# Optimization experiments

Measured on AMD Instinct MI355X. Metric: run time of the kernel, lower is better.

The kernel has to match this reference:

```python
import jax, jax.numpy as jnp
import numpy as np

NUM_HEADS = 16

def setup_inputs() -> dict:
    key = jax.random.key(0)
    k1, k2, k3 = jax.random.split(key, 3)
    B, S, H = 2, 2048, 1024
    x = jax.random.normal(k1, (B, S, H), dtype=jnp.float32)
    w_qkv = jax.random.normal(k2, (H, 3 * H), dtype=jnp.float32) * (1.0 / np.sqrt(H))
    w_out = jax.random.normal(k3, (H, H), dtype=jnp.float32) * (1.0 / np.sqrt(H))
    return {"x": x, "w_qkv": w_qkv, "w_out": w_out}

def reference(x, w_qkv, w_out):
    B, S, H = x.shape
    nh = NUM_HEADS
    dh = H // nh
    qkv = x @ w_qkv  # (B, S, 3H)
    q, k, v = jnp.split(qkv, 3, axis=-1)
    # (B, nh, S, dh)
    q = q.reshape(B, S, nh, dh).transpose(0, 2, 1, 3)
    k = k.reshape(B, S, nh, dh).transpose(0, 2, 1, 3)
    v = v.reshape(B, S, nh, dh).transpose(0, 2, 1, 3)
    att = jnp.einsum('bhsd,bhSd->bhsS', q, k) / np.sqrt(dh).astype(np.float32)
    causal = jnp.tril(jnp.ones((S, S), dtype=bool))
    att = jnp.where(causal[None, None], att, -jnp.inf)
    att = jax.nn.softmax(att, axis=-1)
    out = jnp.einsum('bhsS,bhSd->bhsd', att, v)
    out = out.transpose(0, 2, 1, 3).reshape(B, S, H)
    return out @ w_out
```

## Files before the change

### kernel.cpp

```cpp
#include <hip/hip_runtime.h>

#define DEVINL __device__ __forceinline__

typedef __attribute__((ext_vector_type(8)))  __bf16         bf16x8;
typedef __attribute__((ext_vector_type(4)))  float          f32x4;
typedef __attribute__((ext_vector_type(16))) float          f32x16;
typedef __attribute__((ext_vector_type(8)))  unsigned short ushort8;
typedef __attribute__((ext_vector_type(4)))  unsigned short ushort4v;
typedef __attribute__((ext_vector_type(4)))  unsigned int   uint4v;
typedef __attribute__((ext_vector_type(4)))  float          float4v;

DEVINL unsigned short f2bf(float f) {
  unsigned int u = __float_as_uint(f);
  u += 0x7fffu + ((u >> 16) & 1u);
  return (unsigned short)(u >> 16);
}

DEVINL float bf2f(unsigned short u) {
  return __uint_as_float(((unsigned int)u) << 16);
}

DEVINL bf16x8 ldbf8(const unsigned short* p) {
  return __builtin_bit_cast(bf16x8, *(const ushort8*)p);
}

DEVINL unsigned cvtpk_bf16(float lo, float hi) {
  unsigned r;
  asm("v_cvt_pk_bf16_f32 %0, %1, %2" : "=v"(r) : "v"(lo), "v"(hi));
  return r;
}

DEVINL void gload_lds16(const unsigned short* g, unsigned short* l) {
  __builtin_amdgcn_global_load_lds((const __attribute__((address_space(1))) void*)g,
                                   (__attribute__((address_space(3))) void*)l, 16, 0, 0);
}

__global__ __launch_bounds__(256) void prepass_kernel(
    const float* __restrict__ x, const float* __restrict__ w_qkv,
    const float* __restrict__ w_out, unsigned short* __restrict__ xb,
    unsigned short* __restrict__ wqkvT, unsigned short* __restrict__ woutT) {
  __shared__ float tile[32][33];
  const int B = blockIdx.x;
  if (B < 1024) {
    const int n4 = 1048576;
    for (int i = B * 256 + threadIdx.x; i < n4; i += 1024 * 256) {
      float4v v = *(const float4v*)(x + (size_t)4 * i);
      ushort4v o;
      o[0] = f2bf(v[0]); o[1] = f2bf(v[1]); o[2] = f2bf(v[2]); o[3] = f2bf(v[3]);
      *(ushort4v*)(xb + (size_t)4 * i) = o;
    }
    return;
  }
  const float* in; unsigned short* out; int C, bx, by;
  if (B < 4096) { const int idx = B - 1024; bx = idx % 96; by = idx / 96; in = w_qkv; out = wqkvT; C = 3072; }
  else          { const int idx = B - 4096; bx = idx & 31; by = idx >> 5; in = w_out; out = woutT; C = 1024; }
  const int R = 1024;
  const int tx = threadIdx.x & 31, ty = threadIdx.x >> 5;
  const int r0 = by << 5, c0 = bx << 5;
#pragma unroll
  for (int i = 0; i < 32; i += 8)
    tile[ty + i][tx] = in[(size_t)(r0 + ty + i) * C + (c0 + tx)];
  __syncthreads();
#pragma unroll
  for (int i = 0; i < 32; i += 8)
    out[(size_t)(c0 + ty + i) * R + (r0 + tx)] = f2bf(tile[tx][ty + i]);
}

template <bool OUT_BF16>
__global__ __launch_bounds__(256, 3) void gemm_bt_kernel(
    const unsigned short* __restrict__ A,
    const unsigned short* __restrict__ Bt,
    void* __restrict__ Cout,
    int M, int N, int K, int lda, int ldb, int ldc,
    unsigned short* __restrict__ VtOut) {
  __shared__ __align__(16) unsigned short As[2][128 * 32];
  __shared__ __align__(16) unsigned short Bs[2][128 * 32];
  const int tid = threadIdx.x;
  const int lane = tid & 63, wave = tid >> 6;
  const int wr = wave >> 1, wc = wave & 1;
  const int g = lane >> 4, q = lane & 15;
  const int row0 = blockIdx.x << 7, col0 = blockIdx.y << 7;

  const int srow = tid >> 2;
  const int sg = ((tid & 3) ^ (srow & 3)) << 3;
  const unsigned short* Ap0 = A + (size_t)(row0 + srow) * lda + sg;
  const unsigned short* Ap1 = Ap0 + (size_t)64 * lda;
  const unsigned short* Bp0 = Bt + (size_t)(col0 + srow) * ldb + sg;
  const unsigned short* Bp1 = Bp0 + (size_t)64 * ldb;

  f32x4 acc[4][4] = {};

  gload_lds16(Ap0, &As[0][wave * 512]);
  gload_lds16(Ap1, &As[0][2048 + wave * 512]);
  gload_lds16(Bp0, &Bs[0][wave * 512]);
  gload_lds16(Bp1, &Bs[0][2048 + wave * 512]);

  const int gx = (g ^ (q & 3)) << 3;
  const int nk = K >> 5;
  int cur = 0;

  for (int t = 0; t < nk; ++t) {
    if (t + 1 < nk) {
      Ap0 += 32; Ap1 += 32; Bp0 += 32; Bp1 += 32;
      gload_lds16(Ap0, &As[cur ^ 1][wave * 512]);
      gload_lds16(Ap1, &As[cur ^ 1][2048 + wave * 512]);
      gload_lds16(Bp0, &Bs[cur ^ 1][wave * 512]);
      gload_lds16(Bp1, &Bs[cur ^ 1][2048 + wave * 512]);
      asm volatile("s_waitcnt vmcnt(4)" ::: "memory");
    } else {
      asm volatile("s_waitcnt vmcnt(0)" ::: "memory");
    }
    __builtin_amdgcn_s_barrier();

    bf16x8 af[4], bfr[4];
#pragma unroll
    for (int mb = 0; mb < 4; ++mb)
      af[mb] = ldbf8(&As[cur][(wr * 64 + mb * 16 + q) * 32] + gx);
#pragma unroll
    for (int nb = 0; nb < 4; ++nb)
      bfr[nb] = ldbf8(&Bs[cur][(wc * 64 + nb * 16 + q) * 32] + gx);
#pragma unroll
    for (int mb = 0; mb < 4; ++mb)
#pragma unroll
      for (int nb = 0; nb < 4; ++nb)
        acc[mb][nb] = __builtin_amdgcn_mfma_f32_16x16x32_bf16(af[mb], bfr[nb], acc[mb][nb], 0, 0, 0);

    __builtin_amdgcn_s_barrier();
    cur ^= 1;
  }

  const bool isV = OUT_BF16 && (VtOut != nullptr) && (col0 >= 2048);
#pragma unroll
  for (int mb = 0; mb < 4; ++mb)
#pragma unroll
    for (int nb = 0; nb < 4; ++nb)
#pragma unroll
      for (int r = 0; r < 4; ++r) {
        const int row = row0 + wr * 64 + mb * 16 + g * 4 + r;
        const int col = col0 + wc * 64 + nb * 16 + q;
        const float v = acc[mb][nb][r];
        if (isV) {
          const int cp = col - 2048, hI = cp >> 6, dI = cp & 63;
          VtOut[((size_t)((row >> 11) * 16 + hI) * 64 + dI) * 2048 + (row & 2047)] = f2bf(v);
        } else if (OUT_BF16) {
          ((unsigned short*)Cout)[(size_t)row * ldc + col] = f2bf(v);
        } else {
          ((float*)Cout)[(size_t)row * ldc + col] = v;
        }
      }
}

__global__ __launch_bounds__(256, 3) void gemm_bt64_kernel(
    const unsigned short* __restrict__ A,
    const unsigned short* __restrict__ Bt,
    float* __restrict__ Cout,
    int K, int lda, int ldb, int ldc) {
  __shared__ __align__(16) unsigned short As[2][64 * 32];
  __shared__ __align__(16) unsigned short Bs[2][128 * 32];
  const int tid = threadIdx.x;
  const int lane = tid & 63, wave = tid >> 6;
  const int wr = wave >> 1, wc = wave & 1;
  const int g = lane >> 4, q = lane & 15;
  const int row0 = blockIdx.x << 6, col0 = blockIdx.y << 7;

  const int srow = tid >> 2;
  const int sg = ((tid & 3) ^ (srow & 3)) << 3;
  const unsigned short* Ap = A + (size_t)(row0 + srow) * lda + sg;
  const unsigned short* Bp0 = Bt + (size_t)(col0 + srow) * ldb + sg;
  const unsigned short* Bp1 = Bp0 + (size_t)64 * ldb;

  f32x4 acc[2][4] = {};

  gload_lds16(Ap, &As[0][wave * 512]);
  gload_lds16(Bp0, &Bs[0][wave * 512]);
  gload_lds16(Bp1, &Bs[0][2048 + wave * 512]);

  const int gx = (g ^ (q & 3)) << 3;
  const int nk = K >> 5;
  int cur = 0;

  for (int t = 0; t < nk; ++t) {
    if (t + 1 < nk) {
      Ap += 32; Bp0 += 32; Bp1 += 32;
      gload_lds16(Ap, &As[cur ^ 1][wave * 512]);
      gload_lds16(Bp0, &Bs[cur ^ 1][wave * 512]);
      gload_lds16(Bp1, &Bs[cur ^ 1][2048 + wave * 512]);
      asm volatile("s_waitcnt vmcnt(3)" ::: "memory");
    } else {
      asm volatile("s_waitcnt vmcnt(0)" ::: "memory");
    }
    __builtin_amdgcn_s_barrier();

    bf16x8 af[2], bfr[4];
#pragma unroll
    for (int mb = 0; mb < 2; ++mb)
      af[mb] = ldbf8(&As[cur][(wr * 32 + mb * 16 + q) * 32] + gx);
#pragma unroll
    for (int nb = 0; nb < 4; ++nb)
      bfr[nb] = ldbf8(&Bs[cur][(wc * 64 + nb * 16 + q) * 32] + gx);
#pragma unroll
    for (int mb = 0; mb < 2; ++mb)
#pragma unroll
      for (int nb = 0; nb < 4; ++nb)
        acc[mb][nb] = __builtin_amdgcn_mfma_f32_16x16x32_bf16(af[mb], bfr[nb], acc[mb][nb], 0, 0, 0);

    __builtin_amdgcn_s_barrier();
    cur ^= 1;
  }

#pragma unroll
  for (int mb = 0; mb < 2; ++mb)
#pragma unroll
    for (int nb = 0; nb < 4; ++nb)
#pragma unroll
      for (int r = 0; r < 4; ++r) {
        const int row = row0 + wr * 32 + mb * 16 + g * 4 + r;
        const int col = col0 + wc * 64 + nb * 16 + q;
        Cout[(size_t)row * ldc + col] = acc[mb][nb][r];
      }
}

__global__ __launch_bounds__(256, 2) void attn_kernel(
    const unsigned short* __restrict__ qkv,
    const unsigned short* __restrict__ VtG,
    unsigned short* __restrict__ OlP,
    unsigned short* __restrict__ OhP,
    float* __restrict__ stats) {
  const int S = 2048, H = 1024, LD = 2048;
  const int tid = threadIdx.x;
  const int wave = tid >> 6, lane = tid & 63;
  const int c = lane & 31, hh = lane >> 5;

  const int L = blockIdx.x;
  const int group = L >> 8, r0_ = L & 255;
  const int pairid = r0_ & 7, bh = r0_ >> 3;
  const int qc = (group & 2) ? (15 - pairid) : pairid;
  const int half = group & 1;
  const int b = bh >> 4, h = bh & 15;
  const int q0w = qc * 128 + wave * 32;

  const unsigned short* Qb = qkv + (size_t)b * S * LD + h * 64;
  const unsigned short* Kb = Qb + 1024;
  const unsigned short* Vt = VtG + (size_t)(b * 16 + h) * 64 * S;

  __shared__ __align__(16) unsigned short Ks[2][64 * 64];
  __shared__ __align__(16) unsigned short Vs[2][64 * 64];

  const int srow = lane >> 3;
  const int srcg = ((lane & 7) ^ srow) << 3;
  const int wrow = wave * 8 + srow;

  const int nit = qc + 1;
  const int tb = half ? nit : 0;

  {
    const int cc = tb << 6;
    gload_lds16(Kb + (size_t)(cc + wrow) * LD + srcg,      Ks[0] + wave * 512);
    gload_lds16(Kb + (size_t)(cc + 32 + wrow) * LD + srcg, Ks[0] + 2048 + wave * 512);
    gload_lds16(Vt + (size_t)wrow * S + cc + srcg,         Vs[0] + wave * 512);
    gload_lds16(Vt + (size_t)(32 + wrow) * S + cc + srcg,  Vs[0] + 2048 + wave * 512);
  }

  bf16x8 qf[4];
#pragma unroll
  for (int kc = 0; kc < 4; ++kc)
    qf[kc] = ldbf8(Qb + (size_t)(q0w + c) * LD + kc * 16 + hh * 8);

  f32x16 acc[2] = {};
  float m_r = -1e30f, l_r = 0.f;
  const float CE = 0.125f * 1.44269504f;

  int cur = 0;
  const int swz = (c & 7) << 3;

  for (int t = 0; t < nit; ++t) {
    if (t + 1 < nit) {
      const int c1 = (tb + t + 1) << 6;
      unsigned short* KsN = Ks[cur ^ 1];
      unsigned short* VsN = Vs[cur ^ 1];
      gload_lds16(Kb + (size_t)(c1 + wrow) * LD + srcg,      KsN + wave * 512);
      gload_lds16(Kb + (size_t)(c1 + 32 + wrow) * LD + srcg, KsN + 2048 + wave * 512);
      gload_lds16(Vt + (size_t)wrow * S + c1 + srcg,         VsN + wave * 512);
      gload_lds16(Vt + (size_t)(32 + wrow) * S + c1 + srcg,  VsN + 2048 + wave * 512);
      asm volatile("s_waitcnt vmcnt(4)" ::: "memory");
    } else {
      asm volatile("s_waitcnt vmcnt(0)" ::: "memory");
    }
    __builtin_amdgcn_s_barrier();

    const int c0 = (tb + t) << 6;
    const unsigned short* KsC = Ks[cur];
    const unsigned short* VsC = Vs[cur];

    if (c0 <= q0w + 31) {
      int nv = ((q0w + 31 - c0) >> 5) + 1; if (nv > 2) nv = 2;

      bf16x8 kf[2][4];
#pragma unroll
      for (int n = 0; n < 2; ++n) if (n < nv)
#pragma unroll
        for (int kc = 0; kc < 4; ++kc)
          kf[n][kc] = ldbf8(KsC + (n * 32 + c) * 64 + ((kc * 16 + hh * 8) ^ swz));

      f32x16 st[2] = {};
      __builtin_amdgcn_s_setprio(1);
#pragma unroll
      for (int n = 0; n < 2; ++n) if (n < nv)
#pragma unroll
        for (int kc = 0; kc < 4; ++kc)
          st[n] = __builtin_amdgcn_mfma_f32_32x32x16_bf16(kf[n][kc], qf[kc], st[n], 0, 0, 0);
      __builtin_amdgcn_s_setprio(0);

      bf16x8 vf[2][4];
#pragma unroll
      for (int db = 0; db < 2; ++db)
#pragma unroll
        for (int kk = 0; kk < 4; ++kk) if (kk < 2 * nv)
          vf[db][kk] = ldbf8(VsC + (db * 32 + c) * 64 + ((kk * 16 + hh * 8) ^ swz));

      if (c0 + 63 > q0w) {
#pragma unroll
        for (int n = 0; n < 2; ++n) if (n < nv)
#pragma unroll
          for (int r = 0; r < 16; ++r) {
            const int kv = c0 + n * 32 + (r & 3) + 8 * (r >> 2) + 4 * hh;
            if (kv > q0w + c) st[n][r] = -1e30f;
          }
      }

      f32x4 pm = {-1e30f, -1e30f, -1e30f, -1e30f};
#pragma unroll
      for (int n = 0; n < 2; ++n) if (n < nv)
#pragma unroll
        for (int r = 0; r < 16; ++r) pm[r & 3] = fmaxf(pm[r & 3], st[n][r]);
      const float pmax = fmaxf(fmaxf(pm[0], pm[1]), fmaxf(pm[2], pm[3]));
      if (!__all(pmax <= m_r + 64.f)) {
        float px = fmaxf(pmax, __shfl_xor(pmax, 32));
        const float mn = fmaxf(m_r, px);
        const float sf = __builtin_amdgcn_exp2f((m_r - mn) * CE);
        m_r = mn; l_r *= sf;
#pragma unroll
        for (int db = 0; db < 2; ++db) acc[db] *= sf;
      }
      const float mC = m_r * CE;
      f32x4 la = {0.f, 0.f, 0.f, 0.f};
#pragma unroll
      for (int n = 0; n < 2; ++n) if (n < nv)
#pragma unroll
        for (int r = 0; r < 16; ++r) {
          const float p = __builtin_amdgcn_exp2f(fmaf(st[n][r], CE, -mC));
          st[n][r] = p;
          la[r & 3] += p;
        }
      l_r += (la[0] + la[1]) + (la[2] + la[3]);

      bf16x8 pa[4];
#pragma unroll
      for (int n = 0; n < 2; ++n) if (n < nv) {
        unsigned T0 = cvtpk_bf16(st[n][0],  st[n][1]);
        unsigned T1 = cvtpk_bf16(st[n][2],  st[n][3]);
        unsigned T2 = cvtpk_bf16(st[n][4],  st[n][5]);
        unsigned T3 = cvtpk_bf16(st[n][6],  st[n][7]);
        unsigned T4 = cvtpk_bf16(st[n][8],  st[n][9]);
        unsigned T5 = cvtpk_bf16(st[n][10], st[n][11]);
        unsigned T6 = cvtpk_bf16(st[n][12], st[n][13]);
        unsigned T7 = cvtpk_bf16(st[n][14], st[n][15]);
        asm("v_permlane32_swap_b32 %0, %1" : "+v"(T0), "+v"(T2));
        asm("v_permlane32_swap_b32 %0, %1" : "+v"(T1), "+v"(T3));
        asm("v_permlane32_swap_b32 %0, %1" : "+v"(T4), "+v"(T6));
        asm("v_permlane32_swap_b32 %0, %1" : "+v"(T5), "+v"(T7));
        uint4v w0; w0[0] = T0; w0[1] = T1; w0[2] = T2; w0[3] = T3;
        uint4v w1; w1[0] = T4; w1[1] = T5; w1[2] = T6; w1[3] = T7;
        pa[2 * n]     = __builtin_bit_cast(bf16x8, w0);
        pa[2 * n + 1] = __builtin_bit_cast(bf16x8, w1);
      }

      __builtin_amdgcn_s_setprio(1);
#pragma unroll
      for (int kk = 0; kk < 4; ++kk) if (kk < 2 * nv)
#pragma unroll
        for (int db = 0; db < 2; ++db)
          acc[db] = __builtin_amdgcn_mfma_f32_32x32x16_bf16(vf[db][kk], pa[kk], acc[db], 0, 0, 0);
      __builtin_amdgcn_s_setprio(0);
    }

    __builtin_amdgcn_s_barrier();
    cur ^= 1;
  }

  const float lt = l_r + __shfl_xor(l_r, 32);
  const float inv = lt > 0.f ? 1.f / lt : 0.f;
  unsigned short* Op = half ? OhP : OlP;
  const size_t rowbase = (size_t)(b * S + q0w + c) * H + h * 64;
#pragma unroll
  for (int db = 0; db < 2; ++db)
#pragma unroll
    for (int blk = 0; blk < 4; ++blk) {
      ushort4v o;
#pragma unroll
      for (int j = 0; j < 4; ++j) o[j] = f2bf(acc[db][blk * 4 + j] * inv);
      *(ushort4v*)(Op + rowbase + db * 32 + blk * 8 + hh * 4) = o;
    }
  if (hh == 0) {
    float* sp = stats + ((((size_t)(b * 16 + h)) << 11) + q0w + c) * 4 + (half ? 2 : 0);
    sp[0] = m_r; sp[1] = lt;
  }
}

__global__ __launch_bounds__(256) void attn_merge_kernel(
    const unsigned short* __restrict__ Ol,
    const unsigned short* __restrict__ Oh,
    const float* __restrict__ stats,
    unsigned short* __restrict__ Oout) {
  const float CE = 0.125f * 1.44269504f;
  const int i = blockIdx.x * 256 + threadIdx.x;
  const int r = i >> 7;
  const int g8 = i & 127;
  const int h = g8 >> 3;
  const int s = r & 2047, b = r >> 11;
  const float4v st = *(const float4v*)(stats + ((((size_t)(b * 16 + h)) << 11) + s) * 4);
  const float mn = fmaxf(st[0], st[2]);
  const float wl_ = st[1] * __builtin_amdgcn_exp2f((st[0] - mn) * CE);
  const float wh_ = st[3] * __builtin_amdgcn_exp2f((st[2] - mn) * CE);
  const float inv = 1.f / (wl_ + wh_);
  const float wl = wl_ * inv, wh = wh_ * inv;
  const size_t off = (size_t)i * 8;
  const ushort8 a = *(const ushort8*)(Ol + off);
  const ushort8 cc = *(const ushort8*)(Oh + off);
  ushort8 o;
#pragma unroll
  for (int j = 0; j < 8; ++j)
    o[j] = f2bf(wl * bf2f(a[j]) + wh * bf2f(cc[j]));
  *(ushort8*)(Oout + off) = o;
}

extern "C" void kernel_launch(void* const* d_in, const int* in_sizes, int n_in,
                              void* d_out, int out_size, void* d_ws, size_t ws_size,
                              hipStream_t stream) {
  const float* x     = (const float*)d_in[0];
  const float* w_qkv = (const float*)d_in[1];
  const float* w_out = (const float*)d_in[2];
  const int B = 2, S = 2048, H = 1024;
  const int M = B * S;

  unsigned short* xb    = (unsigned short*)d_ws;
  unsigned short* wqkvT = xb + (size_t)M * H;
  unsigned short* woutT = wqkvT + (size_t)3 * H * H;
  unsigned short* qkb   = woutT + (size_t)H * H;
  unsigned short* VtG   = qkb + (size_t)M * 2048;
  unsigned short* Ob    = VtG + (size_t)B * 16 * 64 * S;
  unsigned short* OhP   = xb;
  float*          stats = (float*)wqkvT;

  prepass_kernel<<<5120, 256, 0, stream>>>(x, w_qkv, w_out, xb, wqkvT, woutT);

  gemm_bt_kernel<true><<<dim3(M / 128, (3 * H) / 128), 256, 0, stream>>>(
      xb, wqkvT, qkb, M, 3 * H, H, H, H, 2048, VtG);

  attn_kernel<<<1024, 256, 0, stream>>>(qkb, VtG, Ob, OhP, stats);

  attn_merge_kernel<<<2048, 256, 0, stream>>>(Ob, OhP, stats, Ob);

  gemm_bt64_kernel<<<dim3(M / 64, H / 128), 256, 0, stream>>>(
      Ob, woutT, (float*)d_out, H, H, H, H);
}
```

Baseline: 116.6 us.

## Load attention K/V fragments directly from global and shrink QKV GEMM tile

The attention kernel stops staging K and V tiles through double-buffered LDS with barriers. Each wave now reads its K and V MFMA fragments straight from global memory and skips fully masked tiles through a tighter loop bound. The QKV projection GEMM switches to the 64-row tile variant, which is merged with the output GEMM into one templated kernel; this doubles the grid and lowers per-block register and LDS use. The trade-off is redundant global/L2 traffic in attention, since waves no longer share K/V tiles, and smaller GEMM tiles that get less operand reuse.

```diff
diff --git a/kernel.cpp b/kernel.cpp
--- a/kernel.cpp
+++ b/kernel.cpp
@@ -67,31 +67,29 @@
 }
 
 template <bool OUT_BF16>
-__global__ __launch_bounds__(256, 3) void gemm_bt_kernel(
+__global__ __launch_bounds__(256, 3) void gemm_bt64_kernel(
     const unsigned short* __restrict__ A,
     const unsigned short* __restrict__ Bt,
     void* __restrict__ Cout,
-    int M, int N, int K, int lda, int ldb, int ldc,
+    int K, int lda, int ldb, int ldc,
     unsigned short* __restrict__ VtOut) {
-  __shared__ __align__(16) unsigned short As[2][128 * 32];
+  __shared__ __align__(16) unsigned short As[2][64 * 32];
   __shared__ __align__(16) unsigned short Bs[2][128 * 32];
   const int tid = threadIdx.x;
   const int lane = tid & 63, wave = tid >> 6;
   const int wr = wave >> 1, wc = wave & 1;
   const int g = lane >> 4, q = lane & 15;
-  const int row0 = blockIdx.x << 7, col0 = blockIdx.y << 7;
+  const int row0 = blockIdx.x << 6, col0 = blockIdx.y << 7;
 
   const int srow = tid >> 2;
   const int sg = ((tid & 3) ^ (srow & 3)) << 3;
-  const unsigned short* Ap0 = A + (size_t)(row0 + srow) * lda + sg;
-  const unsigned short* Ap1 = Ap0 + (size_t)64 * lda;
+  const unsigned short* Ap = A + (size_t)(row0 + srow) * lda + sg;
   const unsigned short* Bp0 = Bt + (size_t)(col0 + srow) * ldb + sg;
   const unsigned short* Bp1 = Bp0 + (size_t)64 * ldb;
 
-  f32x4 acc[4][4] = {};
-
-  gload_lds16(Ap0, &As[0][wave * 512]);
-  gload_lds16(Ap1, &As[0][2048 + wave * 512]);
+  f32x4 acc[2][4] = {};
+
+  gload_lds16(Ap, &As[0][wave * 512]);
   gload_lds16(Bp0, &Bs[0][wave * 512]);
   gload_lds16(Bp1, &Bs[0][2048 + wave * 512]);
 
@@ -101,26 +99,25 @@
 
   for (int t = 0; t < nk; ++t) {
     if (t + 1 < nk) {
-      Ap0 += 32; Ap1 += 32; Bp0 += 32; Bp1 += 32;
-      gload_lds16(Ap0, &As[cur ^ 1][wave * 512]);
-      gload_lds16(Ap1, &As[cur ^ 1][2048 + wave * 512]);
+      Ap += 32; Bp0 += 32; Bp1 += 32;
+      gload_lds16(Ap, &As[cur ^ 1][wave * 512]);
       gload_lds16(Bp0, &Bs[cur ^ 1][wave * 512]);
       gload_lds16(Bp1, &Bs[cur ^ 1][2048 + wave * 512]);
-      asm volatile("s_waitcnt vmcnt(4)" ::: "memory");
+      asm volatile("s_waitcnt vmcnt(3)" ::: "memory");
     } else {
       asm volatile("s_waitcnt vmcnt(0)" ::: "memory");
     }
     __builtin_amdgcn_s_barrier();
 
-    bf16x8 af[4], bfr[4];
-#pragma unroll
-    for (int mb = 0; mb < 4; ++mb)
-      af[mb] = ldbf8(&As[cur][(wr * 64 + mb * 16 + q) * 32] + gx);
+    bf16x8 af[2], bfr[4];
+#pragma unroll
+    for (int mb = 0; mb < 2; ++mb)
+      af[mb] = ldbf8(&As[cur][(wr * 32 + mb * 16 + q) * 32] + gx);
 #pragma unroll
     for (int nb = 0; nb < 4; ++nb)
       bfr[nb] = ldbf8(&Bs[cur][(wc * 64 + nb * 16 + q) * 32] + gx);
 #pragma unroll
-    for (int mb = 0; mb < 4; ++mb)
+    for (int mb = 0; mb < 2; ++mb)
 #pragma unroll
       for (int nb = 0; nb < 4; ++nb)
         acc[mb][nb] = __builtin_amdgcn_mfma_f32_16x16x32_bf16(af[mb], bfr[nb], acc[mb][nb], 0, 0, 0);
@@ -131,12 +128,12 @@
 
   const bool isV = OUT_BF16 && (VtOut != nullptr) && (col0 >= 2048);
 #pragma unroll
-  for (int mb = 0; mb < 4; ++mb)
+  for (int mb = 0; mb < 2; ++mb)
 #pragma unroll
     for (int nb = 0; nb < 4; ++nb)
 #pragma unroll
       for (int r = 0; r < 4; ++r) {
-        const int row = row0 + wr * 64 + mb * 16 + g * 4 + r;
+        const int row = row0 + wr * 32 + mb * 16 + g * 4 + r;
         const int col = col0 + wc * 64 + nb * 16 + q;
         const float v = acc[mb][nb][r];
         if (isV) {
@@ -150,76 +147,6 @@
       }
 }
 
-__global__ __launch_bounds__(256, 3) void gemm_bt64_kernel(
-    const unsigned short* __restrict__ A,
-    const unsigned short* __restrict__ Bt,
-    float* __restrict__ Cout,
-    int K, int lda, int ldb, int ldc) {
-  __shared__ __align__(16) unsigned short As[2][64 * 32];
-  __shared__ __align__(16) unsigned short Bs[2][128 * 32];
-  const int tid = threadIdx.x;
-  const int lane = tid & 63, wave = tid >> 6;
-  const int wr = wave >> 1, wc = wave & 1;
-  const int g = lane >> 4, q = lane & 15;
-  const int row0 = blockIdx.x << 6, col0 = blockIdx.y << 7;
-
-  const int srow = tid >> 2;
-  const int sg = ((tid & 3) ^ (srow & 3)) << 3;
-  const unsigned short* Ap = A + (size_t)(row0 + srow) * lda + sg;
-  const unsigned short* Bp0 = Bt + (size_t)(col0 + srow) * ldb + sg;
-  const unsigned short* Bp1 = Bp0 + (size_t)64 * ldb;
-
-  f32x4 acc[2][4] = {};
-
-  gload_lds16(Ap, &As[0][wave * 512]);
-  gload_lds16(Bp0, &Bs[0][wave * 512]);
-  gload_lds16(Bp1, &Bs[0][2048 + wave * 512]);
-
-  const int gx = (g ^ (q & 3)) << 3;
-  const int nk = K >> 5;
-  int cur = 0;
-
-  for (int t = 0; t < nk; ++t) {
-    if (t + 1 < nk) {
-      Ap += 32; Bp0 += 32; Bp1 += 32;
-      gload_lds16(Ap, &As[cur ^ 1][wave * 512]);
-      gload_lds16(Bp0, &Bs[cur ^ 1][wave * 512]);
-      gload_lds16(Bp1, &Bs[cur ^ 1][2048 + wave * 512]);
-      asm volatile("s_waitcnt vmcnt(3)" ::: "memory");
-    } else {
-      asm volatile("s_waitcnt vmcnt(0)" ::: "memory");
-    }
-    __builtin_amdgcn_s_barrier();
-
-    bf16x8 af[2], bfr[4];
-#pragma unroll
-    for (int mb = 0; mb < 2; ++mb)
-      af[mb] = ldbf8(&As[cur][(wr * 32 + mb * 16 + q) * 32] + gx);
-#pragma unroll
-    for (int nb = 0; nb < 4; ++nb)
-      bfr[nb] = ldbf8(&Bs[cur][(wc * 64 + nb * 16 + q) * 32] + gx);
-#pragma unroll
-    for (int mb = 0; mb < 2; ++mb)
-#pragma unroll
-      for (int nb = 0; nb < 4; ++nb)
-        acc[mb][nb] = __builtin_amdgcn_mfma_f32_16x16x32_bf16(af[mb], bfr[nb], acc[mb][nb], 0, 0, 0);
-
-    __builtin_amdgcn_s_barrier();
-    cur ^= 1;
-  }
-
-#pragma unroll
-  for (int mb = 0; mb < 2; ++mb)
-#pragma unroll
-    for (int nb = 0; nb < 4; ++nb)
-#pragma unroll
-      for (int r = 0; r < 4; ++r) {
-        const int row = row0 + wr * 32 + mb * 16 + g * 4 + r;
-        const int col = col0 + wc * 64 + nb * 16 + q;
-        Cout[(size_t)row * ldc + col] = acc[mb][nb][r];
-      }
-}
-
 __global__ __launch_bounds__(256, 2) void attn_kernel(
     const unsigned short* __restrict__ qkv,
     const unsigned short* __restrict__ VtG,
@@ -243,23 +170,9 @@
   const unsigned short* Kb = Qb + 1024;
   const unsigned short* Vt = VtG + (size_t)(b * 16 + h) * 64 * S;
 
-  __shared__ __align__(16) unsigned short Ks[2][64 * 64];
-  __shared__ __align__(16) unsigned short Vs[2][64 * 64];
-
-  const int srow = lane >> 3;
-  const int srcg = ((lane & 7) ^ srow) << 3;
-  const int wrow = wave * 8 + srow;
-
   const int nit = qc + 1;
   const int tb = half ? nit : 0;
-
-  {
-    const int cc = tb << 6;
-    gload_lds16(Kb + (size_t)(cc + wrow) * LD + srcg,      Ks[0] + wave * 512);
-    gload_lds16(Kb + (size_t)(cc + 32 + wrow) * LD + srcg, Ks[0] + 2048 + wave * 512);
-    gload_lds16(Vt + (size_t)wrow * S + cc + srcg,         Vs[0] + wave * 512);
-    gload_lds16(Vt + (size_t)(32 + wrow) * S + cc + srcg,  Vs[0] + 2048 + wave * 512);
-  }
+  const int te = min(tb + nit, ((q0w + 31) >> 6) + 1);
 
   bf16x8 qf[4];
 #pragma unroll
@@ -270,122 +183,97 @@
   float m_r = -1e30f, l_r = 0.f;
   const float CE = 0.125f * 1.44269504f;
 
-  int cur = 0;
-  const int swz = (c & 7) << 3;
-
-  for (int t = 0; t < nit; ++t) {
-    if (t + 1 < nit) {
-      const int c1 = (tb + t + 1) << 6;
-      unsigned short* KsN = Ks[cur ^ 1];
-      unsigned short* VsN = Vs[cur ^ 1];
-      gload_lds16(Kb + (size_t)(c1 + wrow) * LD + srcg,      KsN + wave * 512);
-      gload_lds16(Kb + (size_t)(c1 + 32 + wrow) * LD + srcg, KsN + 2048 + wave * 512);
-      gload_lds16(Vt + (size_t)wrow * S + c1 + srcg,         VsN + wave * 512);
-      gload_lds16(Vt + (size_t)(32 + wrow) * S + c1 + srcg,  VsN + 2048 + wave * 512);
-      asm volatile("s_waitcnt vmcnt(4)" ::: "memory");
-    } else {
-      asm volatile("s_waitcnt vmcnt(0)" ::: "memory");
-    }
-    __builtin_amdgcn_s_barrier();
-
-    const int c0 = (tb + t) << 6;
-    const unsigned short* KsC = Ks[cur];
-    const unsigned short* VsC = Vs[cur];
-
-    if (c0 <= q0w + 31) {
-      int nv = ((q0w + 31 - c0) >> 5) + 1; if (nv > 2) nv = 2;
-
-      bf16x8 kf[2][4];
+  for (int t = tb; t < te; ++t) {
+    const int c0 = t << 6;
+    int nv = ((q0w + 31 - c0) >> 5) + 1; if (nv > 2) nv = 2;
+
+    bf16x8 kf[2][4];
+#pragma unroll
+    for (int n = 0; n < 2; ++n) if (n < nv)
+#pragma unroll
+      for (int kc = 0; kc < 4; ++kc)
+        kf[n][kc] = ldbf8(Kb + (size_t)(c0 + n * 32 + c) * LD + kc * 16 + hh * 8);
+
+    bf16x8 vf[2][4];
+#pragma unroll
+    for (int db = 0; db < 2; ++db)
+#pragma unroll
+      for (int kk = 0; kk < 4; ++kk) if (kk < 2 * nv)
+        vf[db][kk] = ldbf8(Vt + (size_t)(db * 32 + c) * S + c0 + kk * 16 + hh * 8);
+
+    f32x16 st[2] = {};
+    __builtin_amdgcn_s_setprio(1);
+#pragma unroll
+    for (int n = 0; n < 2; ++n) if (n < nv)
+#pragma unroll
+      for (int kc = 0; kc < 4; ++kc)
+        st[n] = __builtin_amdgcn_mfma_f32_32x32x16_bf16(kf[n][kc], qf[kc], st[n], 0, 0, 0);
+    __builtin_amdgcn_s_setprio(0);
+
+    if (c0 + 63 > q0w) {
 #pragma unroll
       for (int n = 0; n < 2; ++n) if (n < nv)
 #pragma unroll
-        for (int kc = 0; kc < 4; ++kc)
-          kf[n][kc] = ldbf8(KsC + (n * 32 + c) * 64 + ((kc * 16 + hh * 8) ^ swz));
-
-      f32x16 st[2] = {};
-      __builtin_amdgcn_s_setprio(1);
-#pragma unroll
-      for (int n = 0; n < 2; ++n) if (n < nv)
-#pragma unroll
-        for (int kc = 0; kc < 4; ++kc)
-          st[n] = __builtin_amdgcn_mfma_f32_32x32x16_bf16(kf[n][kc], qf[kc], st[n], 0, 0, 0);
-      __builtin_amdgcn_s_setprio(0);
-
-      bf16x8 vf[2][4];
+        for (int r = 0; r < 16; ++r) {
+          const int kv = c0 + n * 32 + (r & 3) + 8 * (r >> 2) + 4 * hh;
+          if (kv > q0w + c) st[n][r] = -1e30f;
+        }
+    }
+
+    f32x4 pm = {-1e30f, -1e30f, -1e30f, -1e30f};
+#pragma unroll
+    for (int n = 0; n < 2; ++n) if (n < nv)
+#pragma unroll
+      for (int r = 0; r < 16; ++r) pm[r & 3] = fmaxf(pm[r & 3], st[n][r]);
+    const float pmax = fmaxf(fmaxf(pm[0], pm[1]), fmaxf(pm[2], pm[3]));
+    if (!__all(pmax <= m_r + 64.f)) {
+      float px = fmaxf(pmax, __shfl_xor(pmax, 32));
+      const float mn = fmaxf(m_r, px);
+      const float sf = __builtin_amdgcn_exp2f((m_r - mn) * CE);
+      m_r = mn; l_r *= sf;
+#pragma unroll
+      for (int db = 0; db < 2; ++db) acc[db] *= sf;
+    }
+    const float mC = m_r * CE;
+    f32x4 la = {0.f, 0.f, 0.f, 0.f};
+#pragma unroll
+    for (int n = 0; n < 2; ++n) if (n < nv)
+#pragma unroll
+      for (int r = 0; r < 16; ++r) {
+        const float p = __builtin_amdgcn_exp2f(fmaf(st[n][r], CE, -mC));
+        st[n][r] = p;
+        la[r & 3] += p;
+      }
+    l_r += (la[0] + la[1]) + (la[2] + la[3]);
+
+    bf16x8 pa[4];
+#pragma unroll
+    for (int n = 0; n < 2; ++n) if (n < nv) {
+      unsigned T0 = cvtpk_bf16(st[n][0],  st[n][1]);
+      unsigned T1 = cvtpk_bf16(st[n][2],  st[n][3]);
+      unsigned T2 = cvtpk_bf16(st[n][4],  st[n][5]);
+      unsigned T3 = cvtpk_bf16(st[n][6],  st[n][7]);
+      unsigned T4 = cvtpk_bf16(st[n][8],  st[n][9]);
+      unsigned T5 = cvtpk_bf16(st[n][10], st[n][11]);
+      unsigned T6 = cvtpk_bf16(st[n][12], st[n][13]);
+      unsigned T7 = cvtpk_bf16(st[n][14], st[n][15]);
+      asm("v_permlane32_swap_b32 %0, %1" : "+v"(T0), "+v"(T2));
+      asm("v_permlane32_swap_b32 %0, %1" : "+v"(T1), "+v"(T3));
+      asm("v_permlane32_swap_b32 %0, %1" : "+v"(T4), "+v"(T6));
+      asm("v_permlane32_swap_b32 %0, %1" : "+v"(T5), "+v"(T7));
+      uint4v w0; w0[0] = T0; w0[1] = T1; w0[2] = T2; w0[3] = T3;
+      uint4v w1; w1[0] = T4; w1[1] = T5; w1[2] = T6; w1[3] = T7;
+      pa[2 * n]     = __builtin_bit_cast(bf16x8, w0);
+      pa[2 * n + 1] = __builtin_bit_cast(bf16x8, w1);
+    }
+
+    __builtin_amdgcn_s_setprio(1);
+#pragma unroll
+    for (int kk = 0; kk < 4; ++kk) if (kk < 2 * nv)
 #pragma unroll
       for (int db = 0; db < 2; ++db)
-#pragma unroll
-        for (int kk = 0; kk < 4; ++kk) if (kk < 2 * nv)
-          vf[db][kk] = ldbf8(VsC + (db * 32 + c) * 64 + ((kk * 16 + hh * 8) ^ swz));
-
-      if (c0 + 63 > q0w) {
-#pragma unroll
-        for (int n = 0; n < 2; ++n) if (n < nv)
-#pragma unroll
-          for (int r = 0; r < 16; ++r) {
-            const int kv = c0 + n * 32 + (r & 3) + 8 * (r >> 2) + 4 * hh;
-            if (kv > q0w + c) st[n][r] = -1e30f;
-          }
-      }
-
-      f32x4 pm = {-1e30f, -1e30f, -1e30f, -1e30f};
-#pragma unroll
-      for (int n = 0; n < 2; ++n) if (n < nv)
-#pragma unroll
-        for (int r = 0; r < 16; ++r) pm[r & 3] = fmaxf(pm[r & 3], st[n][r]);
-      const float pmax = fmaxf(fmaxf(pm[0], pm[1]), fmaxf(pm[2], pm[3]));
-      if (!__all(pmax <= m_r + 64.f)) {
-        float px = fmaxf(pmax, __shfl_xor(pmax, 32));
-        const float mn = fmaxf(m_r, px);
-        const float sf = __builtin_amdgcn_exp2f((m_r - mn) * CE);
-        m_r = mn; l_r *= sf;
-#pragma unroll
-        for (int db = 0; db < 2; ++db) acc[db] *= sf;
-      }
-      const float mC = m_r * CE;
-      f32x4 la = {0.f, 0.f, 0.f, 0.f};
-#pragma unroll
-      for (int n = 0; n < 2; ++n) if (n < nv)
-#pragma unroll
-        for (int r = 0; r < 16; ++r) {
-          const float p = __builtin_amdgcn_exp2f(fmaf(st[n][r], CE, -mC));
-          st[n][r] = p;
-          la[r & 3] += p;
-        }
-      l_r += (la[0] + la[1]) + (la[2] + la[3]);
-
-      bf16x8 pa[4];
-#pragma unroll
-      for (int n = 0; n < 2; ++n) if (n < nv) {
-        unsigned T0 = cvtpk_bf16(st[n][0],  st[n][1]);
-        unsigned T1 = cvtpk_bf16(st[n][2],  st[n][3]);
-        unsigned T2 = cvtpk_bf16(st[n][4],  st[n][5]);
-        unsigned T3 = cvtpk_bf16(st[n][6],  st[n][7]);
-        unsigned T4 = cvtpk_bf16(st[n][8],  st[n][9]);
-        unsigned T5 = cvtpk_bf16(st[n][10], st[n][11]);
-        unsigned T6 = cvtpk_bf16(st[n][12], st[n][13]);
-        unsigned T7 = cvtpk_bf16(st[n][14], st[n][15]);
-        asm("v_permlane32_swap_b32 %0, %1" : "+v"(T0), "+v"(T2));
-        asm("v_permlane32_swap_b32 %0, %1" : "+v"(T1), "+v"(T3));
-        asm("v_permlane32_swap_b32 %0, %1" : "+v"(T4), "+v"(T6));
-        asm("v_permlane32_swap_b32 %0, %1" : "+v"(T5), "+v"(T7));
-        uint4v w0; w0[0] = T0; w0[1] = T1; w0[2] = T2; w0[3] = T3;
-        uint4v w1; w1[0] = T4; w1[1] = T5; w1[2] = T6; w1[3] = T7;
-        pa[2 * n]     = __builtin_bit_cast(bf16x8, w0);
-        pa[2 * n + 1] = __builtin_bit_cast(bf16x8, w1);
-      }
-
-      __builtin_amdgcn_s_setprio(1);
-#pragma unroll
-      for (int kk = 0; kk < 4; ++kk) if (kk < 2 * nv)
-#pragma unroll
-        for (int db = 0; db < 2; ++db)
-          acc[db] = __builtin_amdgcn_mfma_f32_32x32x16_bf16(vf[db][kk], pa[kk], acc[db], 0, 0, 0);
-      __builtin_amdgcn_s_setprio(0);
-    }
-
-    __builtin_amdgcn_s_barrier();
-    cur ^= 1;
+        acc[db] = __builtin_amdgcn_mfma_f32_32x32x16_bf16(vf[db][kk], pa[kk], acc[db], 0, 0, 0);
+    __builtin_amdgcn_s_setprio(0);
   }
 
   const float lt = l_r + __shfl_xor(l_r, 32);
@@ -454,13 +342,13 @@
 
   prepass_kernel<<<5120, 256, 0, stream>>>(x, w_qkv, w_out, xb, wqkvT, woutT);
 
-  gemm_bt_kernel<true><<<dim3(M / 128, (3 * H) / 128), 256, 0, stream>>>(
-      xb, wqkvT, qkb, M, 3 * H, H, H, H, 2048, VtG);
+  gemm_bt64_kernel<true><<<dim3(M / 64, (3 * H) / 128), 256, 0, stream>>>(
+      xb, wqkvT, qkb, H, H, H, 2048, VtG);
 
   attn_kernel<<<1024, 256, 0, stream>>>(qkb, VtG, Ob, OhP, stats);
 
   attn_merge_kernel<<<2048, 256, 0, stream>>>(Ob, OhP, stats, Ob);
 
-  gemm_bt64_kernel<<<dim3(M / 64, H / 128), 256, 0, stream>>>(
-      Ob, woutT, (float*)d_out, H, H, H, H);
-}
+  gemm_bt64_kernel<false><<<dim3(M / 64, H / 128), 256, 0, stream>>>(
+      Ob, woutT, d_out, H, H, H, H, nullptr);
+}
```

Result: slower. 158.9 us (+36.3%).

## Split causal attention KV range into four partials with heavy-first block order

Applied to the files above, without the earlier changes.

Attention blocks now split each query chunk's KV tiles into four quarters instead of two halves. The grid doubles to 2048 blocks and is ordered so the longest causal chunks are scheduled first. The merge kernel now combines four partial outputs using per-quarter max and sum stats, with two of the partial buffers placed in the not-yet-written output buffer. This is meant to cut tail imbalance and raise CU occupancy. In exchange, the merge kernel reads twice as many partial buffers, and some blocks do no work for short chunks.

```diff
diff --git a/kernel.cpp b/kernel.cpp
--- a/kernel.cpp
+++ b/kernel.cpp
@@ -223,8 +223,8 @@
 __global__ __launch_bounds__(256, 2) void attn_kernel(
     const unsigned short* __restrict__ qkv,
     const unsigned short* __restrict__ VtG,
-    unsigned short* __restrict__ OlP,
-    unsigned short* __restrict__ OhP,
+    unsigned short* __restrict__ P0, unsigned short* __restrict__ P1,
+    unsigned short* __restrict__ P2, unsigned short* __restrict__ P3,
     float* __restrict__ stats) {
   const int S = 2048, H = 1024, LD = 2048;
   const int tid = threadIdx.x;
@@ -232,10 +232,10 @@
   const int c = lane & 31, hh = lane >> 5;
 
   const int L = blockIdx.x;
-  const int group = L >> 8, r0_ = L & 255;
-  const int pairid = r0_ & 7, bh = r0_ >> 3;
-  const int qc = (group & 2) ? (15 - pairid) : pairid;
-  const int half = group & 1;
+  const int quarter = L & 3;
+  const int rest = L >> 2;
+  const int bh = rest & 31;
+  const int qc = 15 - (rest >> 5);
   const int b = bh >> 4, h = bh & 15;
   const int q0w = qc * 128 + wave * 32;
 
@@ -250,10 +250,12 @@
   const int srcg = ((lane & 7) ^ srow) << 3;
   const int wrow = wave * 8 + srow;
 
-  const int nit = qc + 1;
-  const int tb = half ? nit : 0;
-
-  {
+  const int T = 2 * qc + 2;
+  const int tb = (T * quarter) >> 2;
+  const int te = (T * (quarter + 1)) >> 2;
+  const int nit = te - tb;
+
+  if (nit > 0) {
     const int cc = tb << 6;
     gload_lds16(Kb + (size_t)(cc + wrow) * LD + srcg,      Ks[0] + wave * 512);
     gload_lds16(Kb + (size_t)(cc + 32 + wrow) * LD + srcg, Ks[0] + 2048 + wave * 512);
@@ -273,9 +275,9 @@
   int cur = 0;
   const int swz = (c & 7) << 3;
 
-  for (int t = 0; t < nit; ++t) {
-    if (t + 1 < nit) {
-      const int c1 = (tb + t + 1) << 6;
+  for (int t = tb; t < te; ++t) {
+    if (t + 1 < te) {
+      const int c1 = (t + 1) << 6;
       unsigned short* KsN = Ks[cur ^ 1];
       unsigned short* VsN = Vs[cur ^ 1];
       gload_lds16(Kb + (size_t)(c1 + wrow) * LD + srcg,      KsN + wave * 512);
@@ -288,7 +290,7 @@
     }
     __builtin_amdgcn_s_barrier();
 
-    const int c0 = (tb + t) << 6;
+    const int c0 = t << 6;
     const unsigned short* KsC = Ks[cur];
     const unsigned short* VsC = Vs[cur];
 
@@ -390,7 +392,7 @@
 
   const float lt = l_r + __shfl_xor(l_r, 32);
   const float inv = lt > 0.f ? 1.f / lt : 0.f;
-  unsigned short* Op = half ? OhP : OlP;
+  unsigned short* Op = (quarter == 0) ? P0 : (quarter == 1) ? P1 : (quarter == 2) ? P2 : P3;
   const size_t rowbase = (size_t)(b * S + q0w + c) * H + h * 64;
 #pragma unroll
   for (int db = 0; db < 2; ++db)
@@ -402,14 +404,14 @@
       *(ushort4v*)(Op + rowbase + db * 32 + blk * 8 + hh * 4) = o;
     }
   if (hh == 0) {
-    float* sp = stats + ((((size_t)(b * 16 + h)) << 11) + q0w + c) * 4 + (half ? 2 : 0);
+    float* sp = stats + ((((size_t)(b * 16 + h)) << 11) + q0w + c) * 8 + quarter * 2;
     sp[0] = m_r; sp[1] = lt;
   }
 }
 
 __global__ __launch_bounds__(256) void attn_merge_kernel(
-    const unsigned short* __restrict__ Ol,
-    const unsigned short* __restrict__ Oh,
+    const unsigned short* __restrict__ P0, const unsigned short* __restrict__ P1,
+    const unsigned short* __restrict__ P2, const unsigned short* __restrict__ P3,
     const float* __restrict__ stats,
     unsigned short* __restrict__ Oout) {
   const float CE = 0.125f * 1.44269504f;
@@ -418,19 +420,25 @@
   const int g8 = i & 127;
   const int h = g8 >> 3;
   const int s = r & 2047, b = r >> 11;
-  const float4v st = *(const float4v*)(stats + ((((size_t)(b * 16 + h)) << 11) + s) * 4);
-  const float mn = fmaxf(st[0], st[2]);
-  const float wl_ = st[1] * __builtin_amdgcn_exp2f((st[0] - mn) * CE);
-  const float wh_ = st[3] * __builtin_amdgcn_exp2f((st[2] - mn) * CE);
-  const float inv = 1.f / (wl_ + wh_);
-  const float wl = wl_ * inv, wh = wh_ * inv;
+  const float* sp = stats + ((((size_t)(b * 16 + h)) << 11) + s) * 8;
+  const float4v s01 = *(const float4v*)sp;
+  const float4v s23 = *(const float4v*)(sp + 4);
+  const float mn = fmaxf(fmaxf(s01[0], s01[2]), fmaxf(s23[0], s23[2]));
+  const float w0 = s01[1] * __builtin_amdgcn_exp2f((s01[0] - mn) * CE);
+  const float w1 = s01[3] * __builtin_amdgcn_exp2f((s01[2] - mn) * CE);
+  const float w2 = s23[1] * __builtin_amdgcn_exp2f((s23[0] - mn) * CE);
+  const float w3 = s23[3] * __builtin_amdgcn_exp2f((s23[2] - mn) * CE);
+  const float inv = 1.f / (w0 + w1 + w2 + w3);
   const size_t off = (size_t)i * 8;
-  const ushort8 a = *(const ushort8*)(Ol + off);
-  const ushort8 cc = *(const ushort8*)(Oh + off);
+  const ushort8 a0 = *(const ushort8*)(P0 + off);
+  const ushort8 a1 = *(const ushort8*)(P1 + off);
+  const ushort8 a2 = *(const ushort8*)(P2 + off);
+  const ushort8 a3 = *(const ushort8*)(P3 + off);
   ushort8 o;
 #pragma unroll
   for (int j = 0; j < 8; ++j)
-    o[j] = f2bf(wl * bf2f(a[j]) + wh * bf2f(cc[j]));
+    o[j] = f2bf((w0 * bf2f(a0[j]) + w1 * bf2f(a1[j]) +
+                 w2 * bf2f(a2[j]) + w3 * bf2f(a3[j])) * inv);
   *(ushort8*)(Oout + off) = o;
 }
 
@@ -449,7 +457,9 @@
   unsigned short* qkb   = woutT + (size_t)H * H;
   unsigned short* VtG   = qkb + (size_t)M * 2048;
   unsigned short* Ob    = VtG + (size_t)B * 16 * 64 * S;
-  unsigned short* OhP   = xb;
+  unsigned short* P1    = xb;
+  unsigned short* P2    = (unsigned short*)d_out;
+  unsigned short* P3    = P2 + (size_t)M * H;
   float*          stats = (float*)wqkvT;
 
   prepass_kernel<<<5120, 256, 0, stream>>>(x, w_qkv, w_out, xb, wqkvT, woutT);
@@ -457,9 +467,9 @@
   gemm_bt_kernel<true><<<dim3(M / 128, (3 * H) / 128), 256, 0, stream>>>(
       xb, wqkvT, qkb, M, 3 * H, H, H, H, 2048, VtG);
 
-  attn_kernel<<<1024, 256, 0, stream>>>(qkb, VtG, Ob, OhP, stats);
-
-  attn_merge_kernel<<<2048, 256, 0, stream>>>(Ob, OhP, stats, Ob);
+  attn_kernel<<<2048, 256, 0, stream>>>(qkb, VtG, Ob, P1, P2, P3, stats);
+
+  attn_merge_kernel<<<2048, 256, 0, stream>>>(Ob, P1, P2, P3, stats, Ob);
 
   gemm_bt64_kernel<<<dim3(M / 64, H / 128), 256, 0, stream>>>(
       Ob, woutT, (float*)d_out, H, H, H, H);
```

Result: slower. 130.9 us (+12.3%).

## Fuse attention split-merge into output projection GEMM and remap QKV block order

Applied to the files above, without the earlier changes.

Removes the separate attn_merge kernel. The output-projection GEMM now loads both partial attention outputs through registers, computes the per-head merge weights from stats, and writes the merged bf16 A tile into LDS itself. This saves one kernel launch and a full write/read round trip of the merged activation. The QKV GEMM also switches to a 1D grid with a remapped block order, likely to change L2 reuse or XCD placement. The cost is that A-tile loads become synchronous register loads plus VALU merge work inside the GEMM main loop, and the merge work is redone once for each of the 8 column blocks.

```diff
diff --git a/kernel.cpp b/kernel.cpp
--- a/kernel.cpp
+++ b/kernel.cpp
@@ -66,11 +66,10 @@
     out[(size_t)(c0 + ty + i) * R + (r0 + tx)] = f2bf(tile[tx][ty + i]);
 }
 
-template <bool OUT_BF16>
-__global__ __launch_bounds__(256, 3) void gemm_bt_kernel(
+__global__ __launch_bounds__(256, 3) void gemm_qkv_kernel(
     const unsigned short* __restrict__ A,
     const unsigned short* __restrict__ Bt,
-    void* __restrict__ Cout,
+    unsigned short* __restrict__ Cout,
     int M, int N, int K, int lda, int ldb, int ldc,
     unsigned short* __restrict__ VtOut) {
   __shared__ __align__(16) unsigned short As[2][128 * 32];
@@ -79,7 +78,10 @@
   const int lane = tid & 63, wave = tid >> 6;
   const int wr = wave >> 1, wc = wave & 1;
   const int g = lane >> 4, q = lane & 15;
-  const int row0 = blockIdx.x << 7, col0 = blockIdx.y << 7;
+  const int bid = blockIdx.x;
+  const int idx = (bid & 7) * 96 + (bid >> 3);
+  const int row0 = (idx & 31) << 7;
+  const int col0 = (idx >> 5) << 7;
 
   const int srow = tid >> 2;
   const int sg = ((tid & 3) ^ (srow & 3)) << 3;
@@ -129,7 +131,7 @@
     cur ^= 1;
   }
 
-  const bool isV = OUT_BF16 && (VtOut != nullptr) && (col0 >= 2048);
+  const bool isV = (col0 >= 2048);
 #pragma unroll
   for (int mb = 0; mb < 4; ++mb)
 #pragma unroll
@@ -142,19 +144,19 @@
         if (isV) {
           const int cp = col - 2048, hI = cp >> 6, dI = cp & 63;
           VtOut[((size_t)((row >> 11) * 16 + hI) * 64 + dI) * 2048 + (row & 2047)] = f2bf(v);
-        } else if (OUT_BF16) {
-          ((unsigned short*)Cout)[(size_t)row * ldc + col] = f2bf(v);
         } else {
-          ((float*)Cout)[(size_t)row * ldc + col] = v;
+          Cout[(size_t)row * ldc + col] = f2bf(v);
         }
       }
 }
 
-__global__ __launch_bounds__(256, 3) void gemm_bt64_kernel(
-    const unsigned short* __restrict__ A,
+__global__ __launch_bounds__(256, 3) void gemm_out_fused_kernel(
+    const unsigned short* __restrict__ Ol,
+    const unsigned short* __restrict__ Oh,
+    const float* __restrict__ stats,
     const unsigned short* __restrict__ Bt,
-    float* __restrict__ Cout,
-    int K, int lda, int ldb, int ldc) {
+    float* __restrict__ Cout) {
+  const float CE = 0.125f * 1.44269504f;
   __shared__ __align__(16) unsigned short As[2][64 * 32];
   __shared__ __align__(16) unsigned short Bs[2][128 * 32];
   const int tid = threadIdx.x;
@@ -165,27 +167,48 @@
 
   const int srow = tid >> 2;
   const int sg = ((tid & 3) ^ (srow & 3)) << 3;
-  const unsigned short* Ap = A + (size_t)(row0 + srow) * lda + sg;
-  const unsigned short* Bp0 = Bt + (size_t)(col0 + srow) * ldb + sg;
-  const unsigned short* Bp1 = Bp0 + (size_t)64 * ldb;
+  const int arow = row0 + srow;
+  const int s = arow & 2047, bb = arow >> 11;
+  const unsigned short* Bp0 = Bt + (size_t)(col0 + srow) * 1024 + sg;
+  const unsigned short* Bp1 = Bp0 + (size_t)64 * 1024;
 
   f32x4 acc[2][4] = {};
 
-  gload_lds16(Ap, &As[0][wave * 512]);
+  size_t aoff = (size_t)arow * 1024 + sg;
+  ushort8 ra = *(const ushort8*)(Ol + aoff);
+  ushort8 rb = *(const ushort8*)(Oh + aoff);
   gload_lds16(Bp0, &Bs[0][wave * 512]);
   gload_lds16(Bp1, &Bs[0][2048 + wave * 512]);
+  float wl, wh;
+  {
+    const float4v sv = *(const float4v*)(stats + ((((size_t)(bb * 16 + 0)) << 11) + s) * 4);
+    const float mn = fmaxf(sv[0], sv[2]);
+    const float a_ = sv[1] * __builtin_amdgcn_exp2f((sv[0] - mn) * CE);
+    const float b_ = sv[3] * __builtin_amdgcn_exp2f((sv[2] - mn) * CE);
+    const float iv = 1.f / (a_ + b_);
+    wl = a_ * iv; wh = b_ * iv;
+  }
+  {
+    ushort8 m8;
+#pragma unroll
+    for (int j = 0; j < 8; ++j) m8[j] = f2bf(wl * bf2f(ra[j]) + wh * bf2f(rb[j]));
+    *(ushort8*)(&As[0][tid * 8]) = m8;
+  }
+  asm volatile("s_waitcnt lgkmcnt(0)" ::: "memory");
 
   const int gx = (g ^ (q & 3)) << 3;
-  const int nk = K >> 5;
+  const int nk = 32;
   int cur = 0;
 
   for (int t = 0; t < nk; ++t) {
     if (t + 1 < nk) {
-      Ap += 32; Bp0 += 32; Bp1 += 32;
-      gload_lds16(Ap, &As[cur ^ 1][wave * 512]);
+      aoff += 32;
+      ra = *(const ushort8*)(Ol + aoff);
+      rb = *(const ushort8*)(Oh + aoff);
+      Bp0 += 32; Bp1 += 32;
       gload_lds16(Bp0, &Bs[cur ^ 1][wave * 512]);
       gload_lds16(Bp1, &Bs[cur ^ 1][2048 + wave * 512]);
-      asm volatile("s_waitcnt vmcnt(3)" ::: "memory");
+      asm volatile("s_waitcnt vmcnt(4)" ::: "memory");
     } else {
       asm volatile("s_waitcnt vmcnt(0)" ::: "memory");
     }
@@ -204,6 +227,22 @@
       for (int nb = 0; nb < 4; ++nb)
         acc[mb][nb] = __builtin_amdgcn_mfma_f32_16x16x32_bf16(af[mb], bfr[nb], acc[mb][nb], 0, 0, 0);
 
+    if (t + 1 < nk) {
+      if (((t + 1) & 1) == 0) {
+        const int hI = (t + 1) >> 1;
+        const float4v sv = *(const float4v*)(stats + ((((size_t)(bb * 16 + hI)) << 11) + s) * 4);
+        const float mn = fmaxf(sv[0], sv[2]);
+        const float a_ = sv[1] * __builtin_amdgcn_exp2f((sv[0] - mn) * CE);
+        const float b_ = sv[3] * __builtin_amdgcn_exp2f((sv[2] - mn) * CE);
+        const float iv = 1.f / (a_ + b_);
+        wl = a_ * iv; wh = b_ * iv;
+      }
+      ushort8 m8;
+#pragma unroll
+      for (int j = 0; j < 8; ++j) m8[j] = f2bf(wl * bf2f(ra[j]) + wh * bf2f(rb[j]));
+      *(ushort8*)(&As[cur ^ 1][tid * 8]) = m8;
+      asm volatile("s_waitcnt lgkmcnt(0)" ::: "memory");
+    }
     __builtin_amdgcn_s_barrier();
     cur ^= 1;
   }
@@ -216,7 +255,7 @@
       for (int r = 0; r < 4; ++r) {
         const int row = row0 + wr * 32 + mb * 16 + g * 4 + r;
         const int col = col0 + wc * 64 + nb * 16 + q;
-        Cout[(size_t)row * ldc + col] = acc[mb][nb][r];
+        Cout[(size_t)row * 1024 + col] = acc[mb][nb][r];
       }
 }
 
@@ -407,33 +446,6 @@
   }
 }
 
-__global__ __launch_bounds__(256) void attn_merge_kernel(
-    const unsigned short* __restrict__ Ol,
-    const unsigned short* __restrict__ Oh,
-    const float* __restrict__ stats,
-    unsigned short* __restrict__ Oout) {
-  const float CE = 0.125f * 1.44269504f;
-  const int i = blockIdx.x * 256 + threadIdx.x;
-  const int r = i >> 7;
-  const int g8 = i & 127;
-  const int h = g8 >> 3;
-  const int s = r & 2047, b = r >> 11;
-  const float4v st = *(const float4v*)(stats + ((((size_t)(b * 16 + h)) << 11) + s) * 4);
-  const float mn = fmaxf(st[0], st[2]);
-  const float wl_ = st[1] * __builtin_amdgcn_exp2f((st[0] - mn) * CE);
-  const float wh_ = st[3] * __builtin_amdgcn_exp2f((st[2] - mn) * CE);
-  const float inv = 1.f / (wl_ + wh_);
-  const float wl = wl_ * inv, wh = wh_ * inv;
-  const size_t off = (size_t)i * 8;
-  const ushort8 a = *(const ushort8*)(Ol + off);
-  const ushort8 cc = *(const ushort8*)(Oh + off);
-  ushort8 o;
-#pragma unroll
-  for (int j = 0; j < 8; ++j)
-    o[j] = f2bf(wl * bf2f(a[j]) + wh * bf2f(cc[j]));
-  *(ushort8*)(Oout + off) = o;
-}
-
 extern "C" void kernel_launch(void* const* d_in, const int* in_sizes, int n_in,
                               void* d_out, int out_size, void* d_ws, size_t ws_size,
                               hipStream_t stream) {
@@ -454,13 +466,11 @@
 
   prepass_kernel<<<5120, 256, 0, stream>>>(x, w_qkv, w_out, xb, wqkvT, woutT);
 
-  gemm_bt_kernel<true><<<dim3(M / 128, (3 * H) / 128), 256, 0, stream>>>(
+  gemm_qkv_kernel<<<768, 256, 0, stream>>>(
       xb, wqkvT, qkb, M, 3 * H, H, H, H, 2048, VtG);
 
   attn_kernel<<<1024, 256, 0, stream>>>(qkb, VtG, Ob, OhP, stats);
 
-  attn_merge_kernel<<<2048, 256, 0, stream>>>(Ob, OhP, stats, Ob);
-
-  gemm_bt64_kernel<<<dim3(M / 64, H / 128), 256, 0, stream>>>(
-      Ob, woutT, (float*)d_out, H, H, H, H);
-}
+  gemm_out_fused_kernel<<<dim3(M / 64, H / 128), 256, 0, stream>>>(
+      Ob, OhP, stats, woutT, (float*)d_out);
+}
```

New measurement: 132.9 us. 1.14x slower.
